# Kernel optimization log

Measured on AMD Instinct MI355X. Metric: run time of the kernel, lower is better.

The kernel has to match this reference:

```python
import jax, jax.numpy as jnp
import numpy as np
from jax import lax

RATIO = 2.0
ITERATIONS = 1


def setup_inputs() -> dict:
    key = jax.random.key(0)
    k1, k2 = jax.random.split(key)
    N, H, W = 64, 512, 512
    x = jax.random.normal(k1, (N, H, W), dtype=jnp.float32)  # logits
    y = jax.random.randint(k2, (N, H, W), 0, 2, dtype=jnp.int32)  # binary labels
    return {"x": x, "y": y}


def _erode(m):
    # cv2.erode with 3x3 all-ones kernel == 3x3 min-pool; cv2 default border
    # value for erode is +inf, matching reduce_window's init_value padding.
    return lax.reduce_window(m, jnp.inf, lax.min, (1, 3, 3), (1, 1, 1), 'SAME')


def _dilate(m):
    # cv2.dilate == 3x3 max-pool; default border value -inf == init_value pad.
    return lax.reduce_window(m, -jnp.inf, lax.max, (1, 3, 3), (1, 1, 1), 'SAME')


def reference(x, y):
    yf = y.astype(x.dtype)
    # elementwise BCE-with-logits (reduction='none'), numerically stable
    loss = jnp.maximum(x, 0.0) - x * yf + jnp.log1p(jnp.exp(-jnp.abs(x)))
    m = (y > 0).astype(x.dtype)  # [N,H,W] binary mask
    ero, dil = m, m
    for _ in range(ITERATIONS):
        ero = _erode(ero)
        dil = _dilate(dil)
    border = dil - ero  # 1 on border pixels, 0 elsewhere
    w = border * RATIO + (1.0 - border)
    return (loss * w).mean()
```

## Files before the change

### kernel.cpp

```cpp
#include <hip/hip_runtime.h>
#include <math.h>

#define NIMG 64
#define HH 512
#define WW 512
#define NBLK 8192
#define INV_TOTAL (1.0f / 16777216.0f)

__global__ __launch_bounds__(256, 8) void border_loss_main(
    const float* __restrict__ x, const int* __restrict__ y,
    float* __restrict__ part, int atomic_mode)
{
    __shared__ float wsum[4];

    const int tid  = threadIdx.x;
    const int idx  = blockIdx.x * 256 + tid;
    const int lane = tid & 63;
    const int r    = (idx >> 6) & (HH - 1);
    const int n    = idx >> 15;
    const int rowb = n * (HH * WW) + r * WW;
    const int col  = lane << 3;

    const int pC = rowb + col;
    const int pT = pC + ((r > 0)      ? -WW : 0);
    const int pB = pC + ((r < HH - 1) ?  WW : 0);

    const int4   t0 = *(const int4*)(y + pT);
    const int4   t1 = *(const int4*)(y + pT + 4);
    const int4   c0 = *(const int4*)(y + pC);
    const int4   c1 = *(const int4*)(y + pC + 4);
    const int4   b0 = *(const int4*)(y + pB);
    const int4   b1 = *(const int4*)(y + pB + 4);
    const float4 xa = *(const float4*)(x + pC);
    const float4 xb = *(const float4*)(x + pC + 4);

    const int vo0 = t0.x | c0.x | b0.x;  const int va0 = t0.x & c0.x & b0.x;
    const int vo1 = t0.y | c0.y | b0.y;  const int va1 = t0.y & c0.y & b0.y;
    const int vo2 = t0.z | c0.z | b0.z;  const int va2 = t0.z & c0.z & b0.z;
    const int vo3 = t0.w | c0.w | b0.w;  const int va3 = t0.w & c0.w & b0.w;
    const int vo4 = t1.x | c1.x | b1.x;  const int va4 = t1.x & c1.x & b1.x;
    const int vo5 = t1.y | c1.y | b1.y;  const int va5 = t1.y & c1.y & b1.y;
    const int vo6 = t1.z | c1.z | b1.z;  const int va6 = t1.z & c1.z & b1.z;
    const int vo7 = t1.w | c1.w | b1.w;  const int va7 = t1.w & c1.w & b1.w;

    const int iL = (lane + 63) & 63, iR = (lane + 1) & 63;
    const int voLs = __shfl(vo7, iL), vaLs = __shfl(va7, iL);
    const int voRs = __shfl(vo0, iR), vaRs = __shfl(va0, iR);
    const int voL = (lane == 0)  ? vo0 : voLs;
    const int vaL = (lane == 0)  ? va0 : vaLs;
    const int voR = (lane == 63) ? vo7 : voRs;
    const int vaR = (lane == 63) ? va7 : vaRs;

    const int ho0 = voL | vo0 | vo1;  const int ha0 = vaL & va0 & va1;
    const int ho1 = vo0 | vo1 | vo2;  const int ha1 = va0 & va1 & va2;
    const int ho2 = vo1 | vo2 | vo3;  const int ha2 = va1 & va2 & va3;
    const int ho3 = vo2 | vo3 | vo4;  const int ha3 = va2 & va3 & va4;
    const int ho4 = vo3 | vo4 | vo5;  const int ha4 = va3 & va4 & va5;
    const int ho5 = vo4 | vo5 | vo6;  const int ha5 = va4 & va5 & va6;
    const int ho6 = vo5 | vo6 | vo7;  const int ha6 = va5 & va6 & va7;
    const int ho7 = vo6 | vo7 | voR;  const int ha7 = va6 & va7 & vaR;

    float acc = 0.0f;
#define PX(xf, m, ho, ha) { \
        const float ls = fmaxf((m) ? -(xf) : (xf), 0.0f) \
                       + __logf(1.0f + __expf(-fabsf(xf))); \
        const float wf = (float)(1 + ((ho) ^ (ha))); \
        acc = fmaf(ls, wf, acc); }
    PX(xa.x, c0.x, ho0, ha0)
    PX(xa.y, c0.y, ho1, ha1)
    PX(xa.z, c0.z, ho2, ha2)
    PX(xa.w, c0.w, ho3, ha3)
    PX(xb.x, c1.x, ho4, ha4)
    PX(xb.y, c1.y, ho5, ha5)
    PX(xb.z, c1.z, ho6, ha6)
    PX(xb.w, c1.w, ho7, ha7)
#undef PX

    #pragma unroll
    for (int off = 32; off > 0; off >>= 1)
        acc += __shfl_down(acc, off);
    if ((tid & 63) == 0) wsum[tid >> 6] = acc;
    __syncthreads();
    if (tid == 0) {
        const float t = wsum[0] + wsum[1] + wsum[2] + wsum[3];
        if (atomic_mode) atomicAdd(part, t * INV_TOTAL);
        else             part[blockIdx.x] = t;
    }
}

__global__ __launch_bounds__(256) void border_loss_reduce(
    const float* __restrict__ part, float* __restrict__ out)
{
    __shared__ float wsum[4];
    float t = 0.0f;
    for (int i = threadIdx.x; i < NBLK; i += 256) t += part[i];
    #pragma unroll
    for (int off = 32; off > 0; off >>= 1)
        t += __shfl_down(t, off);
    if ((threadIdx.x & 63) == 0) wsum[threadIdx.x >> 6] = t;
    __syncthreads();
    if (threadIdx.x == 0)
        out[0] = (wsum[0] + wsum[1] + wsum[2] + wsum[3]) * INV_TOTAL;
}

__global__ void border_loss_zero(float* out) { out[0] = 0.0f; }

extern "C" void kernel_launch(void* const* d_in, const int* in_sizes, int n_in,
                              void* d_out, int out_size, void* d_ws, size_t ws_size,
                              hipStream_t stream)
{
    const float* x = (const float*)d_in[0];
    const int*   y = (const int*)d_in[1];
    float* out = (float*)d_out;

    if (ws_size >= (size_t)NBLK * sizeof(float)) {
        float* part = (float*)d_ws;
        border_loss_main<<<NBLK, 256, 0, stream>>>(x, y, part, 0);
        border_loss_reduce<<<1, 256, 0, stream>>>(part, out);
    } else {
        border_loss_zero<<<1, 1, 0, stream>>>(out);
        border_loss_main<<<NBLK, 256, 0, stream>>>(x, y, out, 1);
    }
}
```

Baseline: 148.5 us.

## Precompute bit-packed label mask and compute border weights with bitwise ops

Adds a pre-pass that packs the binary labels into one bit per pixel. A second kernel then reads x plus three small mask bytes per thread and derives erosion and dilation with shifts and lane shuffles on bit words. This replaces three full int32 row reads of y per pixel with a compact mask, at the cost of an extra kernel launch and a global round trip for the mask. The path is only taken when the workspace is large enough; otherwise the previous fused kernel is used.

```diff
diff --git a/kernel.cpp b/kernel.cpp
--- a/kernel.cpp
+++ b/kernel.cpp
@@ -4,11 +4,29 @@
 #define NIMG 64
 #define HH 512
 #define WW 512
+#define NPIX (NIMG * HH * WW)
 #define NBLK 8192
+#define MASK_BYTES (NPIX / 8)
 #define INV_TOTAL (1.0f / 16777216.0f)
 
-__global__ __launch_bounds__(256, 8) void border_loss_main(
-    const float* __restrict__ x, const int* __restrict__ y,
+typedef unsigned int u32;
+typedef unsigned char u8;
+
+__global__ __launch_bounds__(256, 8) void border_mask_gen(
+    const int* __restrict__ y, u8* __restrict__ mask)
+{
+    const int idx = blockIdx.x * 256 + threadIdx.x;
+    const int4 a = ((const int4*)y)[idx * 2];
+    const int4 b = ((const int4*)y)[idx * 2 + 1];
+    u32 m = (a.x > 0)       | ((a.y > 0) << 1)
+          | ((a.z > 0) << 2) | ((a.w > 0) << 3)
+          | ((b.x > 0) << 4) | ((b.y > 0) << 5)
+          | ((b.z > 0) << 6) | ((b.w > 0) << 7);
+    mask[idx] = (u8)m;
+}
+
+__global__ __launch_bounds__(256, 8) void border_loss_bits(
+    const float* __restrict__ x, const u8* __restrict__ mask,
     float* __restrict__ part, int atomic_mode)
 {
     __shared__ float wsum[4];
@@ -18,9 +36,64 @@
     const int lane = tid & 63;
     const int r    = (idx >> 6) & (HH - 1);
     const int n    = idx >> 15;
+    const int mrC  = (n << 9) | r;
+    const int mrT  = (r > 0)      ? mrC - 1 : mrC;
+    const int mrB  = (r < HH - 1) ? mrC + 1 : mrC;
+
+    const u32 mt = mask[(mrT << 6) + lane];
+    const u32 mc = mask[(mrC << 6) + lane];
+    const u32 mb = mask[(mrB << 6) + lane];
+    const float4 xa = *(const float4*)(x + (idx << 3));
+    const float4 xb = *(const float4*)(x + (idx << 3) + 4);
+
+    const u32 vo = mt | mc | mb;
+    const u32 va = mt & mc & mb;
+
+    const int iL = (lane + 63) & 63, iR = (lane + 1) & 63;
+    const u32 voL = __shfl(vo, iL), vaL = __shfl(va, iL);
+    const u32 voR = __shfl(vo, iR), vaR = __shfl(va, iR);
+    const u32 lbO = (lane == 0)  ? (vo & 1u)        : ((voL >> 7) & 1u);
+    const u32 lbA = (lane == 0)  ? (va & 1u)        : ((vaL >> 7) & 1u);
+    const u32 rbO = (lane == 63) ? ((vo >> 7) & 1u) : (voR & 1u);
+    const u32 rbA = (lane == 63) ? ((va >> 7) & 1u) : (vaR & 1u);
+
+    const u32 ho = vo | ((vo << 1) | lbO) | ((vo >> 1) | (rbO << 7));
+    const u32 ha = va & ((va << 1) | lbA) & ((va >> 1) | (rbA << 7));
+    const u32 bd = ho ^ ha;
+
+    float acc = 0.0f;
+#define PX(xf, k) { \
+        const float ls = fmaxf(((mc >> (k)) & 1u) ? -(xf) : (xf), 0.0f) \
+                       + __logf(1.0f + __expf(-fabsf(xf))); \
+        acc = fmaf(ls, ((bd >> (k)) & 1u) ? 2.0f : 1.0f, acc); }
+    PX(xa.x, 0) PX(xa.y, 1) PX(xa.z, 2) PX(xa.w, 3)
+    PX(xb.x, 4) PX(xb.y, 5) PX(xb.z, 6) PX(xb.w, 7)
+#undef PX
+
+    #pragma unroll
+    for (int off = 32; off > 0; off >>= 1)
+        acc += __shfl_down(acc, off);
+    if ((tid & 63) == 0) wsum[tid >> 6] = acc;
+    __syncthreads();
+    if (tid == 0) {
+        const float t = wsum[0] + wsum[1] + wsum[2] + wsum[3];
+        if (atomic_mode) atomicAdd(part, t * INV_TOTAL);
+        else             part[blockIdx.x] = t;
+    }
+}
+
+__global__ __launch_bounds__(256, 8) void border_loss_fused(
+    const float* __restrict__ x, const int* __restrict__ y,
+    float* __restrict__ part, int atomic_mode)
+{
+    __shared__ float wsum[4];
+    const int tid  = threadIdx.x;
+    const int idx  = blockIdx.x * 256 + tid;
+    const int lane = tid & 63;
+    const int r    = (idx >> 6) & (HH - 1);
+    const int n    = idx >> 15;
     const int rowb = n * (HH * WW) + r * WW;
     const int col  = lane << 3;
-
     const int pC = rowb + col;
     const int pT = pC + ((r > 0)      ? -WW : 0);
     const int pB = pC + ((r < HH - 1) ?  WW : 0);
@@ -64,16 +137,11 @@
 #define PX(xf, m, ho, ha) { \
         const float ls = fmaxf((m) ? -(xf) : (xf), 0.0f) \
                        + __logf(1.0f + __expf(-fabsf(xf))); \
-        const float wf = (float)(1 + ((ho) ^ (ha))); \
-        acc = fmaf(ls, wf, acc); }
-    PX(xa.x, c0.x, ho0, ha0)
-    PX(xa.y, c0.y, ho1, ha1)
-    PX(xa.z, c0.z, ho2, ha2)
-    PX(xa.w, c0.w, ho3, ha3)
-    PX(xb.x, c1.x, ho4, ha4)
-    PX(xb.y, c1.y, ho5, ha5)
-    PX(xb.z, c1.z, ho6, ha6)
-    PX(xb.w, c1.w, ho7, ha7)
+        acc = fmaf(ls, (float)(1 + ((ho) ^ (ha))), acc); }
+    PX(xa.x, c0.x, ho0, ha0) PX(xa.y, c0.y, ho1, ha1)
+    PX(xa.z, c0.z, ho2, ha2) PX(xa.w, c0.w, ho3, ha3)
+    PX(xb.x, c1.x, ho4, ha4) PX(xb.y, c1.y, ho5, ha5)
+    PX(xb.z, c1.z, ho6, ha6) PX(xb.w, c1.w, ho7, ha7)
 #undef PX
 
     #pragma unroll
@@ -113,12 +181,18 @@
     const int*   y = (const int*)d_in[1];
     float* out = (float*)d_out;
 
-    if (ws_size >= (size_t)NBLK * sizeof(float)) {
+    if (ws_size >= (size_t)MASK_BYTES + (size_t)NBLK * sizeof(float)) {
+        u8*    mask = (u8*)d_ws;
+        float* part = (float*)((char*)d_ws + MASK_BYTES);
+        border_mask_gen<<<NBLK, 256, 0, stream>>>(y, mask);
+        border_loss_bits<<<NBLK, 256, 0, stream>>>(x, mask, part, 0);
+        border_loss_reduce<<<1, 256, 0, stream>>>(part, out);
+    } else if (ws_size >= (size_t)NBLK * sizeof(float)) {
         float* part = (float*)d_ws;
-        border_loss_main<<<NBLK, 256, 0, stream>>>(x, y, part, 0);
+        border_loss_fused<<<NBLK, 256, 0, stream>>>(x, y, part, 0);
         border_loss_reduce<<<1, 256, 0, stream>>>(part, out);
     } else {
         border_loss_zero<<<1, 1, 0, stream>>>(out);
-        border_loss_main<<<NBLK, 256, 0, stream>>>(x, y, out, 1);
+        border_loss_fused<<<NBLK, 256, 0, stream>>>(x, y, out, 1);
     }
 }
```

Result: no change. 150.0 us (+1.0%).

## Pack labels into bitmask pass, then compute border loss from bits

Applied to the files above, without the earlier changes.

Adds a first kernel that reads the int32 labels once and packs them into a 1-bit-per-pixel mask in workspace. A second kernel then processes four rows per wave, reading the compact mask for the vertical 3x3 neighbourhood and doing erode/dilate with bitwise shifts. This removes the 3x re-reading of int32 labels for the stencil. It costs an extra kernel launch and a workspace round trip, and swaps the per-block partial-sum reduction kernel for atomicAdd into the output.

```diff
diff --git a/kernel.cpp b/kernel.cpp
--- a/kernel.cpp
+++ b/kernel.cpp
@@ -4,24 +4,120 @@
 #define NIMG 64
 #define HH 512
 #define WW 512
-#define NBLK 8192
+#define NPIX (NIMG * HH * WW)
+#define MASK_BYTES (NPIX / 8)
+#define NBLK_A 8192
+#define NBLK_B 2048
 #define INV_TOTAL (1.0f / 16777216.0f)
 
-__global__ __launch_bounds__(256, 8) void border_loss_main(
-    const float* __restrict__ x, const int* __restrict__ y,
-    float* __restrict__ part, int atomic_mode)
+typedef unsigned int u32;
+typedef unsigned char u8;
+
+__global__ __launch_bounds__(256, 8) void border_mask_gen(
+    const int* __restrict__ y, u8* __restrict__ mask, float* __restrict__ out)
+{
+    const int idx = blockIdx.x * 256 + threadIdx.x;
+    const int4 a = ((const int4*)y)[idx * 2];
+    const int4 b = ((const int4*)y)[idx * 2 + 1];
+    const u32 m = (u32)(a.x > 0)        | ((u32)(a.y > 0) << 1)
+                | ((u32)(a.z > 0) << 2) | ((u32)(a.w > 0) << 3)
+                | ((u32)(b.x > 0) << 4) | ((u32)(b.y > 0) << 5)
+                | ((u32)(b.z > 0) << 6) | ((u32)(b.w > 0) << 7);
+    mask[idx] = (u8)m;
+    if (idx == 0) out[0] = 0.0f;
+}
+
+__global__ __launch_bounds__(256, 8) void border_loss_bits(
+    const float* __restrict__ x, const u8* __restrict__ mask,
+    float* __restrict__ out)
 {
     __shared__ float wsum[4];
 
+    const int tid  = threadIdx.x;
+    const int lane = tid & 63;
+    const int wid  = blockIdx.x * 4 + (tid >> 6);
+    const int r0   = wid << 2;
+    const int n    = r0 >> 9;
+    const int ir0  = r0 & (HH - 1);
+    const int mb   = (n << 15) + lane;
+
+#define IRJ(j) (min(max(ir0 - 1 + (j), 0), HH - 1))
+    const u32 m0 = mask[mb + (IRJ(0) << 6)];
+    const u32 m1 = mask[mb + (IRJ(1) << 6)];
+    const u32 m2 = mask[mb + (IRJ(2) << 6)];
+    const u32 m3 = mask[mb + (IRJ(3) << 6)];
+    const u32 m4 = mask[mb + (IRJ(4) << 6)];
+    const u32 m5 = mask[mb + (IRJ(5) << 6)];
+#undef IRJ
+
+    const float* xp = x + r0 * WW + (lane << 3);
+    const float4 x0a = *(const float4*)(xp);
+    const float4 x0b = *(const float4*)(xp + 4);
+    const float4 x1a = *(const float4*)(xp + WW);
+    const float4 x1b = *(const float4*)(xp + WW + 4);
+    const float4 x2a = *(const float4*)(xp + 2 * WW);
+    const float4 x2b = *(const float4*)(xp + 2 * WW + 4);
+    const float4 x3a = *(const float4*)(xp + 3 * WW);
+    const float4 x3b = *(const float4*)(xp + 3 * WW + 4);
+
+    const u32 M  = m1 | (m2 << 8) | (m3 << 16) | (m4 << 24);
+    const u32 VO = (m0 | m1 | m2)         | ((m1 | m2 | m3) << 8)
+                 | ((m2 | m3 | m4) << 16) | ((m3 | m4 | m5) << 24);
+    const u32 VA = (m0 & m1 & m2)         | ((m1 & m2 & m3) << 8)
+                 | ((m2 & m3 & m4) << 16) | ((m3 & m4 & m5) << 24);
+
+    const int iL = (lane + 63) & 63, iR = (lane + 1) & 63;
+    const u32 VOLs = __shfl(VO, iL), VALs = __shfl(VA, iL);
+    const u32 VORs = __shfl(VO, iR), VARs = __shfl(VA, iR);
+    const u32 lbO = (lane == 0)  ? (VO & 0x01010101u) : ((VOLs >> 7) & 0x01010101u);
+    const u32 lbA = (lane == 0)  ? (VA & 0x01010101u) : ((VALs >> 7) & 0x01010101u);
+    const u32 rbO = (lane == 63) ? (VO & 0x80808080u) : ((VORs & 0x01010101u) << 7);
+    const u32 rbA = (lane == 63) ? (VA & 0x80808080u) : ((VARs & 0x01010101u) << 7);
+
+    const u32 HO = VO | (((VO << 1) & 0xFEFEFEFEu) | lbO)
+                      | (((VO >> 1) & 0x7F7F7F7Fu) | rbO);
+    const u32 HA = VA & (((VA << 1) & 0xFEFEFEFEu) | lbA)
+                      & (((VA >> 1) & 0x7F7F7F7Fu) | rbA);
+    const u32 BD = HO ^ HA;
+
+    float acc = 0.0f;
+#define PX(xf, bi) { \
+        const float ls = fmaxf(((M >> (bi)) & 1u) ? -(xf) : (xf), 0.0f) \
+                       + __logf(1.0f + __expf(-fabsf(xf))); \
+        acc = fmaf(ls, ((BD >> (bi)) & 1u) ? 2.0f : 1.0f, acc); }
+    PX(x0a.x,  0) PX(x0a.y,  1) PX(x0a.z,  2) PX(x0a.w,  3)
+    PX(x0b.x,  4) PX(x0b.y,  5) PX(x0b.z,  6) PX(x0b.w,  7)
+    PX(x1a.x,  8) PX(x1a.y,  9) PX(x1a.z, 10) PX(x1a.w, 11)
+    PX(x1b.x, 12) PX(x1b.y, 13) PX(x1b.z, 14) PX(x1b.w, 15)
+    PX(x2a.x, 16) PX(x2a.y, 17) PX(x2a.z, 18) PX(x2a.w, 19)
+    PX(x2b.x, 20) PX(x2b.y, 21) PX(x2b.z, 22) PX(x2b.w, 23)
+    PX(x3a.x, 24) PX(x3a.y, 25) PX(x3a.z, 26) PX(x3a.w, 27)
+    PX(x3b.x, 28) PX(x3b.y, 29) PX(x3b.z, 30) PX(x3b.w, 31)
+#undef PX
+
+    #pragma unroll
+    for (int off = 32; off > 0; off >>= 1)
+        acc += __shfl_down(acc, off);
+    if (lane == 0) wsum[tid >> 6] = acc;
+    __syncthreads();
+    if (tid == 0) {
+        const float t = wsum[0] + wsum[1] + wsum[2] + wsum[3];
+        atomicAdd(out, t * INV_TOTAL);
+    }
+}
+
+__global__ __launch_bounds__(256, 8) void border_loss_fused(
+    const float* __restrict__ x, const int* __restrict__ y,
+    float* __restrict__ out)
+{
+    __shared__ float wsum[4];
     const int tid  = threadIdx.x;
     const int idx  = blockIdx.x * 256 + tid;
     const int lane = tid & 63;
     const int r    = (idx >> 6) & (HH - 1);
     const int n    = idx >> 15;
     const int rowb = n * (HH * WW) + r * WW;
-    const int col  = lane << 3;
-
-    const int pC = rowb + col;
+    const int pC = rowb + (lane << 3);
     const int pT = pC + ((r > 0)      ? -WW : 0);
     const int pB = pC + ((r < HH - 1) ?  WW : 0);
 
@@ -44,12 +140,10 @@
     const int vo7 = t1.w | c1.w | b1.w;  const int va7 = t1.w & c1.w & b1.w;
 
     const int iL = (lane + 63) & 63, iR = (lane + 1) & 63;
-    const int voLs = __shfl(vo7, iL), vaLs = __shfl(va7, iL);
-    const int voRs = __shfl(vo0, iR), vaRs = __shfl(va0, iR);
-    const int voL = (lane == 0)  ? vo0 : voLs;
-    const int vaL = (lane == 0)  ? va0 : vaLs;
-    const int voR = (lane == 63) ? vo7 : voRs;
-    const int vaR = (lane == 63) ? va7 : vaRs;
+    const int voL = (lane == 0)  ? vo0 : __shfl(vo7, iL);
+    const int vaL = (lane == 0)  ? va0 : __shfl(va7, iL);
+    const int voR = (lane == 63) ? vo7 : __shfl(vo0, iR);
+    const int vaR = (lane == 63) ? va7 : __shfl(va0, iR);
 
     const int ho0 = voL | vo0 | vo1;  const int ha0 = vaL & va0 & va1;
     const int ho1 = vo0 | vo1 | vo2;  const int ha1 = va0 & va1 & va2;
@@ -64,43 +158,22 @@
 #define PX(xf, m, ho, ha) { \
         const float ls = fmaxf((m) ? -(xf) : (xf), 0.0f) \
                        + __logf(1.0f + __expf(-fabsf(xf))); \
-        const float wf = (float)(1 + ((ho) ^ (ha))); \
-        acc = fmaf(ls, wf, acc); }
-    PX(xa.x, c0.x, ho0, ha0)
-    PX(xa.y, c0.y, ho1, ha1)
-    PX(xa.z, c0.z, ho2, ha2)
-    PX(xa.w, c0.w, ho3, ha3)
-    PX(xb.x, c1.x, ho4, ha4)
-    PX(xb.y, c1.y, ho5, ha5)
-    PX(xb.z, c1.z, ho6, ha6)
-    PX(xb.w, c1.w, ho7, ha7)
+        acc = fmaf(ls, (float)(1 + ((ho) ^ (ha))), acc); }
+    PX(xa.x, c0.x, ho0, ha0) PX(xa.y, c0.y, ho1, ha1)
+    PX(xa.z, c0.z, ho2, ha2) PX(xa.w, c0.w, ho3, ha3)
+    PX(xb.x, c1.x, ho4, ha4) PX(xb.y, c1.y, ho5, ha5)
+    PX(xb.z, c1.z, ho6, ha6) PX(xb.w, c1.w, ho7, ha7)
 #undef PX
 
     #pragma unroll
     for (int off = 32; off > 0; off >>= 1)
         acc += __shfl_down(acc, off);
-    if ((tid & 63) == 0) wsum[tid >> 6] = acc;
+    if (lane == 0) wsum[tid >> 6] = acc;
     __syncthreads();
     if (tid == 0) {
         const float t = wsum[0] + wsum[1] + wsum[2] + wsum[3];
-        if (atomic_mode) atomicAdd(part, t * INV_TOTAL);
-        else             part[blockIdx.x] = t;
+        atomicAdd(out, t * INV_TOTAL);
     }
-}
-
-__global__ __launch_bounds__(256) void border_loss_reduce(
-    const float* __restrict__ part, float* __restrict__ out)
-{
-    __shared__ float wsum[4];
-    float t = 0.0f;
-    for (int i = threadIdx.x; i < NBLK; i += 256) t += part[i];
-    #pragma unroll
-    for (int off = 32; off > 0; off >>= 1)
-        t += __shfl_down(t, off);
-    if ((threadIdx.x & 63) == 0) wsum[threadIdx.x >> 6] = t;
-    __syncthreads();
-    if (threadIdx.x == 0)
-        out[0] = (wsum[0] + wsum[1] + wsum[2] + wsum[3]) * INV_TOTAL;
 }
 
 __global__ void border_loss_zero(float* out) { out[0] = 0.0f; }
@@ -113,12 +186,12 @@
     const int*   y = (const int*)d_in[1];
     float* out = (float*)d_out;
 
-    if (ws_size >= (size_t)NBLK * sizeof(float)) {
-        float* part = (float*)d_ws;
-        border_loss_main<<<NBLK, 256, 0, stream>>>(x, y, part, 0);
-        border_loss_reduce<<<1, 256, 0, stream>>>(part, out);
+    if (ws_size >= (size_t)MASK_BYTES) {
+        u8* mask = (u8*)d_ws;
+        border_mask_gen<<<NBLK_A, 256, 0, stream>>>(y, mask, out);
+        border_loss_bits<<<NBLK_B, 256, 0, stream>>>(x, mask, out);
     } else {
         border_loss_zero<<<1, 1, 0, stream>>>(out);
-        border_loss_main<<<NBLK, 256, 0, stream>>>(x, y, out, 1);
+        border_loss_fused<<<NBLK_A, 256, 0, stream>>>(x, y, out);
     }
 }
```

After: 155.7 us. 4.9% more time.
